# Kernel optimization log

Hardware: AMD Instinct MI355X
Metric: run time of the kernel (lower is better)

The kernel has to match this reference:

```python
import jax, jax.numpy as jnp
import numpy as np
from jax import lax

B, C, H, W = 8, 256, 128, 128


def _scan_along(x, decay, axis):
    """Linear decay recurrence s_t = decay*s_{t-1} + (1-decay)*x_t along `axis`.

    x: [B, C, H, W]; decay: [C] (constant per channel).
    """
    xm = jnp.moveaxis(x, axis, 0)          # [L, B, C, rest]
    d = decay.reshape(1, -1, 1)            # broadcast over [B, C, rest]
    one_minus_d = 1.0 - d

    def step(state, cur):
        state = d * state + one_minus_d * cur
        return state, state

    init = jnp.zeros_like(xm[0])
    _, ys = lax.scan(step, init, xm)
    return jnp.moveaxis(ys, 0, axis)


def setup_inputs() -> dict:
    key = jax.random.key(0)
    k1, k2, k3, k4 = jax.random.split(key, 4)
    x = jax.random.normal(k1, (B, C, H, W), dtype=jnp.float32)
    decay_logits = 0.5 * jax.random.normal(k2, (4, C), dtype=jnp.float32)
    mix_logits = 0.5 * jax.random.normal(k3, (4, C), dtype=jnp.float32)
    input_scale = 0.5 * jax.random.normal(k4, (4, C), dtype=jnp.float32)
    return {"x": x, "decay_logits": decay_logits,
            "mix_logits": mix_logits, "input_scale": input_scale}


def reference(x, decay_logits, mix_logits, input_scale):
    decay = jnp.clip(jax.nn.sigmoid(decay_logits), 0.05, 0.995)   # [4, C]
    mix = jax.nn.softmax(mix_logits, axis=0)                       # [4, C]
    scale = 1.0 + jnp.tanh(input_scale)                            # [4, C]

    def sc(d):  # per-channel [C] -> broadcastable [1, C, 1, 1]
        return d.reshape(1, -1, 1, 1)

    # left -> right: scan along width (axis 3)
    lr = _scan_along(x * sc(scale[0]), decay[0], axis=3)
    # right -> left: flip width, scan, flip back
    rl = jnp.flip(_scan_along(jnp.flip(x, axis=3) * sc(scale[1]), decay[1], axis=3), axis=3)
    # top -> bottom: scan along height (axis 2)
    tb = _scan_along(x * sc(scale[2]), decay[2], axis=2)
    # bottom -> top: flip height, scan, flip back
    bt = jnp.flip(_scan_along(jnp.flip(x, axis=2) * sc(scale[3]), decay[3], axis=2), axis=2)

    return sc(mix[0]) * lr + sc(mix[1]) * rl + sc(mix[2]) * tb + sc(mix[3]) * bt
```

## Files before the change

kernel.cpp:

```cpp
#include <hip/hip_runtime.h>

#define CH 256
#define HH 128
#define WW 128
#define HW (HH * WW)
#define SEGH 16
#define NSEG 8

__device__ __forceinline__ float rdlane(float v, int l) {
    return __int_as_float(__builtin_amdgcn_readlane(__float_as_int(v), l));
}
__device__ __forceinline__ float uni(float v) {
    return __int_as_float(__builtin_amdgcn_readfirstlane(__float_as_int(v)));
}

__global__ __launch_bounds__(1024, 2) void dscan_kernel(
    const float* __restrict__ x,
    const float* __restrict__ decay_logits,
    const float* __restrict__ mix_logits,
    const float* __restrict__ input_scale,
    float* __restrict__ out)
{
    extern __shared__ float smem[];
    float* __restrict__ xs  = smem;
    float* __restrict__ scr = smem + HW;

    const int img  = blockIdx.x;
    const int c    = img & (CH - 1);
    const int tid  = threadIdx.x;
    const int lane = tid & 63;

    float pv = 0.0f;
    {
        const int j = lane & 3;
        const int g = lane >> 2;
        if (g == 0) {
            const float v = decay_logits[j * CH + c];
            pv = fminf(fmaxf(1.0f / (1.0f + expf(-v)), 0.05f), 0.995f);
        } else if (g == 1) {
            const float a0 = mix_logits[0 * CH + c];
            const float a1 = mix_logits[1 * CH + c];
            const float a2 = mix_logits[2 * CH + c];
            const float a3 = mix_logits[3 * CH + c];
            const float mm = fmaxf(fmaxf(a0, a1), fmaxf(a2, a3));
            const float aj = (j == 0) ? a0 : (j == 1) ? a1 : (j == 2) ? a2 : a3;
            pv = expf(aj - mm);
        } else if (g == 2) {
            pv = 1.0f + tanhf(input_scale[j * CH + c]);
        }
    }
    const float d0 = rdlane(pv, 0), d1 = rdlane(pv, 1);
    const float d2 = rdlane(pv, 2), d3 = rdlane(pv, 3);
    const float e0 = rdlane(pv, 4), e1 = rdlane(pv, 5);
    const float e2 = rdlane(pv, 6), e3 = rdlane(pv, 7);
    const float s0 = rdlane(pv, 8), s1 = rdlane(pv, 9);
    const float s2 = rdlane(pv, 10), s3 = rdlane(pv, 11);

    const float einv = uni(1.0f / (e0 + e1 + e2 + e3));
    const float m0 = uni(e0 * einv), m1 = uni(e1 * einv);
    const float m2 = uni(e2 * einv), m3 = uni(e3 * einv);
    const float c0 = uni((1.0f - d0) * s0);
    const float c1 = uni((1.0f - d1) * s1);
    const float c2 = uni((1.0f - d2) * s2);
    const float c3 = uni((1.0f - d3) * s3);

    float q0[3], q1[3];
    {
        float a = d0 * d0; a = a * a; a = a * a; a = a * a;
        q0[0] = uni(a); q0[1] = uni(q0[0] * q0[0]); q0[2] = uni(q0[1] * q0[1]);
        float b = d1 * d1; b = b * b; b = b * b; b = b * b;
        q1[0] = uni(b); q1[1] = uni(q1[0] * q1[0]); q1[2] = uni(q1[1] * q1[1]);
    }
    float t2v = d2 * d2; t2v = t2v * t2v; t2v = t2v * t2v; const float d2p16 = uni(t2v * t2v);
    float t3v = d3 * d3; t3v = t3v * t3v; t3v = t3v * t3v; const float d3p16 = uni(t3v * t3v);

    const float* __restrict__ xg = x + (size_t)img * HW;
    float* __restrict__ og = out + (size_t)img * HW;

    {
        const int hr = tid >> 3;
        const int hk = tid & 7;

        const float* __restrict__ xrow = xg + hr * WW + hk * 16;
        const float4 a0 = *(const float4*)(xrow + 0);
        const float4 a1 = *(const float4*)(xrow + 4);
        const float4 a2 = *(const float4*)(xrow + 8);
        const float4 a3 = *(const float4*)(xrow + 12);
        float xr[16];
        xr[0]=a0.x;  xr[1]=a0.y;  xr[2]=a0.z;  xr[3]=a0.w;
        xr[4]=a1.x;  xr[5]=a1.y;  xr[6]=a1.z;  xr[7]=a1.w;
        xr[8]=a2.x;  xr[9]=a2.y;  xr[10]=a2.z; xr[11]=a2.w;
        xr[12]=a3.x; xr[13]=a3.y; xr[14]=a3.z; xr[15]=a3.w;

        float bL = c0 * xr[0];
#pragma unroll
        for (int i = 1; i < 16; ++i) bL = fmaf(d0, bL, c0 * xr[i]);
        float bR = c1 * xr[15];
#pragma unroll
        for (int i = 14; i >= 0; --i) bR = fmaf(d1, bR, c1 * xr[i]);

#pragma unroll
        for (int kk = 0; kk < 3; ++kk) {
            const int off = 1 << kk;
            const float bU = __shfl_up(bL, (unsigned)off, 8);
            bL = fmaf(q0[kk], (hk >= off) ? bU : 0.0f, bL);
            const float bD = __shfl_down(bR, (unsigned)off, 8);
            bR = fmaf(q1[kk], (hk < 8 - off) ? bD : 0.0f, bR);
        }
        float EL = __shfl_up(bL, 1u, 8);
        if (hk == 0) EL = 0.0f;
        float ER = __shfl_down(bR, 1u, 8);
        if (hk == 7) ER = 0.0f;

        float rr[16];
        float t = ER;
#pragma unroll
        for (int i = 15; i >= 0; --i) { t = fmaf(d1, t, c1 * xr[i]); rr[i] = t; }

        float l = EL;
        float* __restrict__ prow = xs + hr * WW + hk * 16;
        const int rsw = hr & 3;
#pragma unroll
        for (int j = 0; j < 4; ++j) {
            float4 o4;
            l = fmaf(d0, l, c0 * xr[4*j + 0]); o4.x = fmaf(m0, l, m1 * rr[4*j + 0]);
            l = fmaf(d0, l, c0 * xr[4*j + 1]); o4.y = fmaf(m0, l, m1 * rr[4*j + 1]);
            l = fmaf(d0, l, c0 * xr[4*j + 2]); o4.z = fmaf(m0, l, m1 * rr[4*j + 2]);
            l = fmaf(d0, l, c0 * xr[4*j + 3]); o4.w = fmaf(m0, l, m1 * rr[4*j + 3]);
            *(float4*)(prow + 4 * (j ^ rsw)) = o4;
        }
    }

    const int col = tid & (WW - 1);
    const int seg = tid >> 7;
    const float* __restrict__ xcol = xg + seg * SEGH * WW + col;

    float xv[SEGH];
#pragma unroll
    for (int i = 0; i < SEGH; ++i) xv[i] = xcol[i * WW];

    {
        float b2 = 0.0f;
#pragma unroll
        for (int i = 0; i < SEGH; ++i) b2 = fmaf(d2, b2, c2 * xv[i]);

        float b3 = 0.0f;
#pragma unroll
        for (int i = SEGH - 1; i >= 0; --i) b3 = fmaf(d3, b3, xv[i]);
        b3 *= c3;

        scr[tid]        = b2;
        scr[1024 + tid] = b3;
    }

    __syncthreads();

    float Sin = 0.0f;
    for (int j = 0; j < seg; ++j)
        Sin = fmaf(d2p16, Sin, scr[j * WW + col]);
    float Tin = 0.0f;
    for (int j = NSEG - 1; j > seg; --j)
        Tin = fmaf(d3p16, Tin, scr[1024 + j * WW + col]);

    {
        const int rbase = seg * SEGH;
        float o[SEGH];
        float s = Sin;
#pragma unroll
        for (int i = 0; i < SEGH; ++i) {
            s = fmaf(d2, s, c2 * xv[i]);
            const float h = xs[(rbase + i) * WW + (col ^ ((i & 3) << 2))];
            o[i] = fmaf(m2, s, h);
        }
        float t = Tin;
        float* __restrict__ ocol = og + rbase * WW + col;
#pragma unroll
        for (int i = SEGH - 1; i >= 0; --i) {
            t = fmaf(d3, t, c3 * xv[i]);
            ocol[i * WW] = fmaf(m3, t, o[i]);
        }
    }
}

extern "C" void kernel_launch(void* const* d_in, const int* in_sizes, int n_in,
                              void* d_out, int out_size, void* d_ws, size_t ws_size,
                              hipStream_t stream) {
    const float* x  = (const float*)d_in[0];
    const float* dl = (const float*)d_in[1];
    const float* ml = (const float*)d_in[2];
    const float* is = (const float*)d_in[3];
    float* out = (float*)d_out;

    const size_t lds_bytes = (size_t)(HW + 2048) * sizeof(float);

    static bool attr_set = false;
    if (!attr_set) {
        (void)hipFuncSetAttribute((const void*)dscan_kernel,
                                  hipFuncAttributeMaxDynamicSharedMemorySize,
                                  (int)lds_bytes);
        attr_set = true;
    }

    dim3 grid(2048), block(1024);
    hipLaunchKernelGGL(dscan_kernel, grid, block, lds_bytes, stream, x, dl, ml, is, out);
}
```

Baseline: 242.2 us.

## Split row block-sums, hoist column loads, and re-swizzle LDS layout

Each 16-wide row block-sum is split into two independent 8-element chains combined with d^8, which shortens the serial FMA dependency. The column loads of x are hoisted into the row phase so their global latency overlaps the shuffle prefix computation. The LDS swizzle for the horizontal partial results changes to a per-column fixed offset, so the column read no longer needs a per-row XOR. The launch-bounds min-blocks hint is raised to 8, which may tighten the register budget and cause spills, since the LDS size already limits occupancy.

New measurement: 240.9 us. Within noise of the previous version (-0.5%).

```diff
diff --git a/kernel.cpp b/kernel.cpp
--- a/kernel.cpp
+++ b/kernel.cpp
@@ -14,7 +14,7 @@
     return __int_as_float(__builtin_amdgcn_readfirstlane(__float_as_int(v)));
 }
 
-__global__ __launch_bounds__(1024, 2) void dscan_kernel(
+__global__ __launch_bounds__(1024, 8) void dscan_kernel(
     const float* __restrict__ x,
     const float* __restrict__ decay_logits,
     const float* __restrict__ mix_logits,
@@ -64,18 +64,25 @@
     const float c2 = uni((1.0f - d2) * s2);
     const float c3 = uni((1.0f - d3) * s3);
 
-    float q0[3], q1[3];
-    {
-        float a = d0 * d0; a = a * a; a = a * a; a = a * a;
-        q0[0] = uni(a); q0[1] = uni(q0[0] * q0[0]); q0[2] = uni(q0[1] * q0[1]);
-        float b = d1 * d1; b = b * b; b = b * b; b = b * b;
-        q1[0] = uni(b); q1[1] = uni(q1[0] * q1[0]); q1[2] = uni(q1[1] * q1[1]);
+    float p8_0, p8_1, q0[3], q1[3];
+    {
+        float a = d0 * d0; a = a * a;
+        p8_0 = uni(a * a);
+        q0[0] = uni(p8_0 * p8_0); q0[1] = uni(q0[0] * q0[0]); q0[2] = uni(q0[1] * q0[1]);
+        float b = d1 * d1; b = b * b;
+        p8_1 = uni(b * b);
+        q1[0] = uni(p8_1 * p8_1); q1[1] = uni(q1[0] * q1[0]); q1[2] = uni(q1[1] * q1[1]);
     }
     float t2v = d2 * d2; t2v = t2v * t2v; t2v = t2v * t2v; const float d2p16 = uni(t2v * t2v);
     float t3v = d3 * d3; t3v = t3v * t3v; t3v = t3v * t3v; const float d3p16 = uni(t3v * t3v);
 
     const float* __restrict__ xg = x + (size_t)img * HW;
     float* __restrict__ og = out + (size_t)img * HW;
+
+    const int col = tid & (WW - 1);
+    const int seg = tid >> 7;
+    const float* __restrict__ xcol = xg + seg * SEGH * WW + col;
+    float xv[SEGH];
 
     {
         const int hr = tid >> 3;
@@ -92,12 +99,24 @@
         xr[8]=a2.x;  xr[9]=a2.y;  xr[10]=a2.z; xr[11]=a2.w;
         xr[12]=a3.x; xr[13]=a3.y; xr[14]=a3.z; xr[15]=a3.w;
 
-        float bL = c0 * xr[0];
-#pragma unroll
-        for (int i = 1; i < 16; ++i) bL = fmaf(d0, bL, c0 * xr[i]);
-        float bR = c1 * xr[15];
-#pragma unroll
-        for (int i = 14; i >= 0; --i) bR = fmaf(d1, bR, c1 * xr[i]);
+        float blo = c0 * xr[0];
+#pragma unroll
+        for (int i = 1; i < 8; ++i)  blo = fmaf(d0, blo, c0 * xr[i]);
+        float bhi = c0 * xr[8];
+#pragma unroll
+        for (int i = 9; i < 16; ++i) bhi = fmaf(d0, bhi, c0 * xr[i]);
+        float bL = fmaf(p8_0, blo, bhi);
+
+        float rA = c1 * xr[15];
+#pragma unroll
+        for (int i = 14; i >= 8; --i) rA = fmaf(d1, rA, c1 * xr[i]);
+        float rB = c1 * xr[7];
+#pragma unroll
+        for (int i = 6; i >= 0; --i)  rB = fmaf(d1, rB, c1 * xr[i]);
+        float bR = fmaf(p8_1, rA, rB);
+
+#pragma unroll
+        for (int i = 0; i < SEGH; ++i) xv[i] = xcol[i * WW];
 
 #pragma unroll
         for (int kk = 0; kk < 3; ++kk) {
@@ -118,8 +137,7 @@
         for (int i = 15; i >= 0; --i) { t = fmaf(d1, t, c1 * xr[i]); rr[i] = t; }
 
         float l = EL;
-        float* __restrict__ prow = xs + hr * WW + hk * 16;
-        const int rsw = hr & 3;
+        float* __restrict__ prow = xs + hr * WW;
 #pragma unroll
         for (int j = 0; j < 4; ++j) {
             float4 o4;
@@ -127,17 +145,9 @@
             l = fmaf(d0, l, c0 * xr[4*j + 1]); o4.y = fmaf(m0, l, m1 * rr[4*j + 1]);
             l = fmaf(d0, l, c0 * xr[4*j + 2]); o4.z = fmaf(m0, l, m1 * rr[4*j + 2]);
             l = fmaf(d0, l, c0 * xr[4*j + 3]); o4.w = fmaf(m0, l, m1 * rr[4*j + 3]);
-            *(float4*)(prow + 4 * (j ^ rsw)) = o4;
-        }
-    }
-
-    const int col = tid & (WW - 1);
-    const int seg = tid >> 7;
-    const float* __restrict__ xcol = xg + seg * SEGH * WW + col;
-
-    float xv[SEGH];
-#pragma unroll
-    for (int i = 0; i < SEGH; ++i) xv[i] = xcol[i * WW];
+            *(float4*)(prow + 4 * ((hk ^ (2*j)) + 8*j)) = o4;
+        }
+    }
 
     {
         float b2 = 0.0f;
@@ -164,13 +174,17 @@
 
     {
         const int rbase = seg * SEGH;
+        const int hkc = col >> 4;
+        const int jc  = (col >> 2) & 3;
+        const int off = 4 * ((hkc ^ (2*jc)) + 8*jc) + (col & 3);
+        const float* __restrict__ pcol = xs + rbase * WW + off;
+
         float o[SEGH];
         float s = Sin;
 #pragma unroll
         for (int i = 0; i < SEGH; ++i) {
             s = fmaf(d2, s, c2 * xv[i]);
-            const float h = xs[(rbase + i) * WW + (col ^ ((i & 3) << 2))];
-            o[i] = fmaf(m2, s, h);
+            o[i] = fmaf(m2, s, pcol[i * WW]);
         }
         float t = Tin;
         float* __restrict__ ocol = og + rbase * WW + col;
```
